# Performance work log

Hardware: AMD Instinct MI355X
Metric: run time of the kernel (lower is better)

The kernel has to match this reference:

```python
import jax, jax.numpy as jnp
import numpy as np

N = 4096      # sequence length (tokens)
D = 256       # model_dim
H = 4         # num_heads
DH = D // H   # dim_per_head = 64
TOPK = 30     # dot_attention default
SCALE = float((DH // H) ** -0.5)  # torch: (key.size(-1)//num_heads)**-0.5 = 16**-0.5 = 0.25
LN_EPS = 1e-5


def setup_inputs() -> dict:
    key = jax.random.key(0)
    ks = jax.random.split(key, 11)
    s = 0.02
    return {
        "key_in":   jax.random.normal(ks[0], (N, D), jnp.float32),
        "value_in": jax.random.normal(ks[1], (N, D), jnp.float32),
        "query_in": jax.random.normal(ks[2], (N, D), jnp.float32),
        "Wq": jax.random.normal(ks[3], (D, D), jnp.float32) * s,
        "bq": jax.random.normal(ks[4], (D,), jnp.float32) * s,
        "Wk": jax.random.normal(ks[5], (D, D), jnp.float32) * s,
        "bk": jax.random.normal(ks[6], (D,), jnp.float32) * s,
        "Wv": jax.random.normal(ks[7], (D, D), jnp.float32) * s,
        "bv": jax.random.normal(ks[8], (D,), jnp.float32) * s,
        "Wo": jax.random.normal(ks[9], (D, D), jnp.float32) * s,
        "bo": jax.random.normal(ks[10], (D,), jnp.float32) * s,
        "ln_g": jnp.ones((D,), jnp.float32),
        "ln_b": jnp.zeros((D,), jnp.float32),
    }


def reference(key_in, value_in, query_in, Wq, bq, Wk, bk, Wv, bv, Wo, bo, ln_g, ln_b):
    # Projections (nn.Linear: x @ W.T + b)
    q = query_in @ Wq.T + bq            # (N, D)
    k = key_in @ Wk.T + bk
    v = value_in @ Wv.T + bv
    # view(N, H, DH).transpose(0,1) -> (H, N, DH)
    qh = q.reshape(N, H, DH).transpose(1, 0, 2)
    kh = k.reshape(N, H, DH).transpose(1, 0, 2)
    vh = v.reshape(N, H, DH).transpose(1, 0, 2)

    scores = jnp.einsum('hnd,hmd->hnm', qh, kh) * SCALE   # (H, N, N)

    # top-k mask via scatter (faithful to torch.topk + scatter_)
    idx = jax.lax.top_k(scores, TOPK)[1]                  # (H, N, TOPK)
    mask = jnp.zeros_like(scores).at[
        jnp.arange(H)[:, None, None],
        jnp.arange(N)[None, :, None],
        idx].set(1.0)
    masked = jnp.where(mask > 0, scores, -jnp.inf)
    attn = jax.nn.softmax(masked, axis=-1)                # (H, N, N); dropout p=0 -> identity

    ctx = jnp.einsum('hnm,hmd->hnd', attn, vh)            # (H, N, DH)
    ctx = ctx.transpose(1, 0, 2).reshape(N, D)

    out = ctx @ Wo.T + bo
    resid = query_in + out                                # residual is pre-projection query
    mu = resid.mean(axis=-1, keepdims=True)
    var = resid.var(axis=-1, keepdims=True)               # biased var, like torch LayerNorm
    out = (resid - mu) / jnp.sqrt(var + LN_EPS) * ln_g + ln_b
    return out, attn
```

## Files before the change

### kernel.cpp

```cpp
#include <hip/hip_runtime.h>
#include <stdint.h>

#define N_TOK 4096
#define DIM   256
#define NH    4
#define DH    64
#define TOPK  30
#define CANDN 40
#define HWIN  128u
#define ATT_SCALE 0.25f
#define LN_EPS 1e-5f

typedef __attribute__((ext_vector_type(8))) short bf16x8;
typedef __attribute__((ext_vector_type(4))) float f32x4;

static __device__ __forceinline__ ushort f2bf(float f) {
    uint x = __float_as_uint(f);
    return (ushort)((x + 0x7FFFu + ((x >> 16) & 1u)) >> 16);
}
static __device__ __forceinline__ bf16x8 load_frag(const ushort* p) {
    union { int4 i; bf16x8 f; } u;
    u.i = *reinterpret_cast<const int4*>(p);
    return u.f;
}
static __device__ __forceinline__ uint s16key(uint u) {
    return (u & 0x8000u) ? (u ^ 0xFFFFu) : (u | 0x8000u);
}
static __device__ __forceinline__ int jdecode(int P) {
    return (P & ~127) | ((P & 7) << 4) | ((P >> 3) & 15);
}

#define BK 32
__global__ __launch_bounds__(256) void qk_gemm_f32(
    const float* __restrict__ query_in, const float* __restrict__ key_in,
    const float* __restrict__ Wq, const float* __restrict__ bq,
    const float* __restrict__ Wk, const float* __restrict__ bk,
    float* __restrict__ qf, float* __restrict__ kf,
    ushort* __restrict__ qb, ushort* __restrict__ kb)
{
    const int j0g = blockIdx.x * 64;
    const int sel = j0g >> 8;
    const int j0  = j0g & 255;
    const float* A    = sel ? key_in : query_in;
    const float* W    = sel ? Wk : Wq;
    const float* bias = sel ? bk : bq;
    float*  outF = sel ? kf : qf;
    ushort* outB = sel ? kb : qb;

    __shared__ float As[BK][64 + 4];
    __shared__ float Ws[BK][64 + 4];
    const int tid = threadIdx.x;
    const int tx = tid & 15;
    const int ty = tid >> 4;
    const int i0 = blockIdx.y * 64;

    float acc[4][4];
#pragma unroll
    for (int r = 0; r < 4; r++)
#pragma unroll
        for (int c = 0; c < 4; c++) acc[r][c] = 0.f;

    for (int k0 = 0; k0 < DIM; k0 += BK) {
#pragma unroll
        for (int u = 0; u < 2; u++) {
            const int f = u * 256 + tid;
            const int r = f >> 3;
            const int c = (f & 7) * 4;
            float4 va = *reinterpret_cast<const float4*>(A + (size_t)(i0 + r) * DIM + k0 + c);
            As[c + 0][r] = va.x; As[c + 1][r] = va.y;
            As[c + 2][r] = va.z; As[c + 3][r] = va.w;
            float4 vw = *reinterpret_cast<const float4*>(W + (size_t)(j0 + r) * DIM + k0 + c);
            Ws[c + 0][r] = vw.x; Ws[c + 1][r] = vw.y;
            Ws[c + 2][r] = vw.z; Ws[c + 3][r] = vw.w;
        }
        __syncthreads();
#pragma unroll
        for (int kk = 0; kk < BK; kk++) {
            const float4 a4 = *reinterpret_cast<const float4*>(&As[kk][ty * 4]);
            const float4 b4 = *reinterpret_cast<const float4*>(&Ws[kk][tx * 4]);
            const float ar[4] = {a4.x, a4.y, a4.z, a4.w};
            const float br[4] = {b4.x, b4.y, b4.z, b4.w};
#pragma unroll
            for (int r = 0; r < 4; r++)
#pragma unroll
                for (int c = 0; c < 4; c++) acc[r][c] += ar[r] * br[c];
        }
        __syncthreads();
    }

#pragma unroll
    for (int r = 0; r < 4; r++) {
        const int gi = i0 + ty * 4 + r;
#pragma unroll
        for (int c = 0; c < 4; c++) {
            const int gj = j0 + tx * 4 + c;
            float v = acc[r][c] + bias[gj];
            outF[(size_t)gi * DIM + gj] = v;
            outB[(size_t)gi * DIM + gj] = f2bf(v);
        }
    }
}

__global__ __launch_bounds__(256) void cast_kernel(
    const float* __restrict__ value_in, const float* __restrict__ Wv,
    const float* __restrict__ Wo, ushort* __restrict__ value_b,
    ushort* __restrict__ Wv_b, ushort* __restrict__ Wo_b)
{
    const int id4 = blockIdx.x * 256 + threadIdx.x;
    const int NV = 1048576 / 4, NW = 65536 / 4;
    const float* src; ushort* dst; int off;
    if (id4 < NV)            { src = value_in; dst = value_b; off = id4; }
    else if (id4 < NV + NW)  { src = Wv; dst = Wv_b; off = id4 - NV; }
    else                     { src = Wo; dst = Wo_b; off = id4 - NV - NW; }
    float4 v = reinterpret_cast<const float4*>(src)[off];
    ushort4 o = {f2bf(v.x), f2bf(v.y), f2bf(v.z), f2bf(v.w)};
    reinterpret_cast<ushort4*>(dst)[off] = o;
}

__global__ __launch_bounds__(256) void mfma_gemm(
    const ushort* __restrict__ A, const ushort* __restrict__ B,
    const float* __restrict__ bias, const float* __restrict__ addX,
    float* __restrict__ outF)
{
    const int lane = threadIdx.x & 63;
    const int wv   = threadIdx.x >> 6;
    const int i0   = blockIdx.y * 64 + wv * 16;
    const int j0   = blockIdx.x * 64;
    const int r = lane & 15, q = lane >> 4;

    f32x4 acc[4];
#pragma unroll
    for (int b = 0; b < 4; b++) acc[b] = (f32x4){0.f, 0.f, 0.f, 0.f};

#pragma unroll
    for (int ks = 0; ks < 8; ks++) {
        const int kk = ks * 32 + q * 8;
        bf16x8 af = load_frag(A + (size_t)(i0 + r) * DIM + kk);
        bf16x8 bfr[4];
#pragma unroll
        for (int jt = 0; jt < 4; jt++)
            bfr[jt] = load_frag(B + (size_t)(j0 + jt * 16 + r) * DIM + kk);
#pragma unroll
        for (int jt = 0; jt < 4; jt++)
            acc[jt] = __builtin_amdgcn_mfma_f32_16x16x32_bf16(af, bfr[jt], acc[jt], 0, 0, 0);
    }

#pragma unroll
    for (int jt = 0; jt < 4; jt++) {
        const int gj = j0 + jt * 16 + r;
        const float bv = bias[gj];
#pragma unroll
        for (int rg = 0; rg < 4; rg++) {
            const int gi = i0 + q * 4 + rg;
            float v = acc[jt][rg] + bv;
            if (addX) v += addX[(size_t)gi * DIM + gj];
            outF[(size_t)gi * DIM + gj] = v;
        }
    }
}

__global__ __launch_bounds__(256) void scores_kernel(
    const ushort* __restrict__ qb, const ushort* __restrict__ kb,
    ushort* __restrict__ sb)
{
    const int lane = threadIdx.x & 63;
    const int wv   = threadIdx.x >> 6;
    const int h    = blockIdx.z;
    const int i0   = blockIdx.y * 128 + wv * 32;
    const int j0   = blockIdx.x * 128;
    const int r = lane & 15, q = lane >> 4;
    const int koff = h * DH;

    f32x4 acc[2][8];
#pragma unroll
    for (int a = 0; a < 2; a++)
#pragma unroll
        for (int b = 0; b < 8; b++) acc[a][b] = (f32x4){0.f, 0.f, 0.f, 0.f};

#pragma unroll
    for (int ks = 0; ks < 2; ks++) {
        const int kk = koff + ks * 32 + q * 8;
        bf16x8 af[2], bfr[8];
#pragma unroll
        for (int mt = 0; mt < 2; mt++)
            af[mt] = load_frag(qb + (size_t)(i0 + mt * 16 + r) * DIM + kk);
#pragma unroll
        for (int jt = 0; jt < 8; jt++)
            bfr[jt] = load_frag(kb + (size_t)(j0 + jt * 16 + r) * DIM + kk);
#pragma unroll
        for (int mt = 0; mt < 2; mt++)
#pragma unroll
            for (int jt = 0; jt < 8; jt++)
                acc[mt][jt] = __builtin_amdgcn_mfma_f32_16x16x32_bf16(
                    af[mt], bfr[jt], acc[mt][jt], 0, 0, 0);
    }

    const int tileBase = (j0 >> 7) * 16;
#pragma unroll
    for (int mt = 0; mt < 2; mt++)
#pragma unroll
        for (int rg = 0; rg < 4; rg++) {
            const int gi = i0 + mt * 16 + q * 4 + rg;
            uint w4[4];
#pragma unroll
            for (int p = 0; p < 4; p++) {
                const uint klo = s16key(f2bf(acc[mt][2 * p + 0][rg]));
                const uint khi = s16key(f2bf(acc[mt][2 * p + 1][rg]));
                w4[p] = klo | (khi << 16);
            }
            int4 outv;
            outv.x = (int)w4[0]; outv.y = (int)w4[1];
            outv.z = (int)w4[2]; outv.w = (int)w4[3];
            int4* rowp = reinterpret_cast<int4*>(sb + ((size_t)(h * N_TOK + gi)) * N_TOK);
            rowp[tileBase + r] = outv;
        }
}

__global__ __launch_bounds__(256) void select_kernel(
    const ushort* __restrict__ sb, const float* __restrict__ qf,
    const float* __restrict__ kf, const float* __restrict__ vf,
    float* __restrict__ pval, int* __restrict__ pidx,
    ushort* __restrict__ ctxb)
{
    const int lane = threadIdx.x & 63;
    const int wv   = threadIdx.x >> 6;
    const int row  = blockIdx.x * 4 + wv;
    const int h    = row >> 12;
    const int i    = row & (N_TOK - 1);
    const ushort* srow = sb + (size_t)row * N_TOK;

    __shared__ uint  hist[4][256];
    __shared__ uint  cand[4][64];
    __shared__ uint  ccnt[4];
    __shared__ float pw[4][TOPK];
    __shared__ int   jw[4][TOPK];
    __shared__ __align__(16) float qsh[4][DH];

    qsh[wv][lane] = qf[(size_t)i * DIM + h * DH + lane];
    if (lane == 0) ccnt[wv] = 0;
#pragma unroll
    for (int b = 0; b < 4; b++) hist[wv][b * 64 + lane] = 0u;

    uint kw[32];
    const int4* srow4 = reinterpret_cast<const int4*>(srow);
#pragma unroll
    for (int t = 0; t < 8; t++) {
        int4 c = srow4[t * 64 + lane];
        kw[t * 4 + 0] = (uint)c.x; kw[t * 4 + 1] = (uint)c.y;
        kw[t * 4 + 2] = (uint)c.z; kw[t * 4 + 3] = (uint)c.w;
    }

    uint mx = 0;
#pragma unroll
    for (int w = 0; w < 32; w++) {
        uint lo16 = kw[w] & 0xFFFFu, hi16 = kw[w] >> 16;
        mx = max(mx, max(lo16, hi16));
    }
#pragma unroll
    for (int off = 32; off; off >>= 1)
        mx = max(mx, (uint)__shfl_xor((int)mx, off));

    __syncthreads();

#pragma unroll
    for (int w = 0; w < 32; w++) {
        uint d0 = mx - (kw[w] & 0xFFFFu);
        uint d1 = mx - (kw[w] >> 16);
        if (d0 < HWIN) atomicAdd(&hist[wv][d0], 1u);
        if (d1 < HWIN) atomicAdd(&hist[wv][d1], 1u);
    }
    __syncthreads();

    const uint c0 = hist[wv][lane * 4 + 0];
    const uint c1 = hist[wv][lane * 4 + 1];
    const uint c2 = hist[wv][lane * 4 + 2];
    const uint c3 = hist[wv][lane * 4 + 3];
    const uint seg = c0 + c1 + c2 + c3;
    uint scan = seg;
#pragma unroll
    for (int d = 1; d < 64; d <<= 1) {
        uint y = (uint)__shfl_up((int)scan, d);
        if (lane >= d) scan += y;
    }
    const uint excl = scan - seg;
    const bool crossing = (excl < CANDN) && (scan >= CANDN);
    unsigned long long bal = __ballot(crossing);

    int t = 256;
    if (bal != 0ull) {
        const int srcLane = __ffsll(bal) - 1;
        int tloc = lane * 4;
        if (crossing) {
            uint cum = excl + c0;
            if (cum < CANDN) { tloc++; cum += c1;
                if (cum < CANDN) { tloc++; cum += c2;
                    if (cum < CANDN) { tloc++; } } }
        }
        t = __shfl(tloc, srcLane);
    }

    uint T;
    if (t <= 254) {
        T = mx - (uint)t;
    } else {
        uint lo = 0;
#pragma unroll
        for (int b = 15; b >= 0; b--) {
            uint trial = lo | (1u << b);
            int c = 0;
#pragma unroll
            for (int w = 0; w < 32; w++) {
                c += ((kw[w] & 0xFFFFu) >= trial) ? 1 : 0;
                c += ((kw[w] >> 16)     >= trial) ? 1 : 0;
            }
#pragma unroll
            for (int off = 32; off; off >>= 1) c += __shfl_xor(c, off);
            if (c >= CANDN) lo = trial;
        }
        T = lo;
    }

#pragma unroll
    for (int w = 0; w < 32; w++) {
        const uint lo16 = kw[w] & 0xFFFFu, hi16 = kw[w] >> 16;
        const int P0 = (w >> 2) * 512 + lane * 8 + (w & 3) * 2;
        if (lo16 >= T) {
            uint pos = atomicAdd(&ccnt[wv], 1u);
            if (pos < 64u) cand[wv][pos] = (uint)jdecode(P0);
        }
        if (hi16 >= T) {
            uint pos = atomicAdd(&ccnt[wv], 1u);
            if (pos < 64u) cand[wv][pos] = (uint)jdecode(P0 + 1);
        }
    }
    __syncthreads();
    const int m = (int)min(ccnt[wv], 64u);

    unsigned long long ukey = 0ull;
    if (lane < m) {
        const int j = (int)cand[wv][lane];
        const float4* kr = reinterpret_cast<const float4*>(kf + (size_t)j * DIM + h * DH);
        const float4* qr = reinterpret_cast<const float4*>(qsh[wv]);
        float s = 0.f;
#pragma unroll
        for (int d = 0; d < 16; d++) {
            float4 a = qr[d], bb = kr[d];
            s += a.x * bb.x; s += a.y * bb.y; s += a.z * bb.z; s += a.w * bb.w;
        }
        uint bits = __float_as_uint(s);
        uint s32 = (bits & 0x80000000u) ? ~bits : (bits | 0x80000000u);
        ukey = ((unsigned long long)s32 << 12) | (unsigned long long)(4095 - j);
    }

#pragma unroll
    for (int k = 2; k <= 64; k <<= 1) {
#pragma unroll
        for (int jj = k >> 1; jj > 0; jj >>= 1) {
            unsigned long long o = __shfl_xor(ukey, jj);
            bool keepMax = ((lane & jj) != 0) ^ ((lane & k) != 0);
            ukey = keepMax ? (ukey > o ? ukey : o) : (ukey < o ? ukey : o);
        }
    }

    const int rank = 63 - lane;
    const int jsel = 4095 - (int)(ukey & 0xFFFull);
    uint s32b = (uint)(ukey >> 12);
    uint fb = (s32b & 0x80000000u) ? (s32b ^ 0x80000000u) : ~s32b;
    const float sc = __uint_as_float(fb);
    const float stop = __shfl(sc, 63);

    float e = (rank < TOPK) ? __expf((sc - stop) * ATT_SCALE) : 0.f;
    float esum = e;
#pragma unroll
    for (int off = 32; off; off >>= 1) esum += __shfl_xor(esum, off);
    const float p = e / esum;

    if (rank < TOPK) {
        pw[wv][rank] = p; jw[wv][rank] = jsel;
        pval[(size_t)row * 32 + rank] = p;
        pidx[(size_t)row * 32 + rank] = jsel;
    }
    __syncthreads();

    float a = 0.f;
#pragma unroll
    for (int c = 0; c < TOPK; c++)
        a += pw[wv][c] * vf[(size_t)jw[wv][c] * DIM + h * DH + lane];
    ctxb[(size_t)i * DIM + h * DH + lane] = f2bf(a);
}

__global__ __launch_bounds__(256) void attn_write(
    const float* __restrict__ pval, const int* __restrict__ pidx,
    float* __restrict__ attnF)
{
    __shared__ __align__(16) float rb[4][N_TOK];
    const int tid = threadIdx.x;
    const int r0 = blockIdx.x * 4;

    float4* rb4 = reinterpret_cast<float4*>(&rb[0][0]);
    const float4 z = {0.f, 0.f, 0.f, 0.f};
#pragma unroll
    for (int t = 0; t < 16; t++) rb4[t * 256 + tid] = z;
    __syncthreads();
    if (tid < 4 * TOPK) {
        const int w = tid / TOPK, c = tid % TOPK;
        rb[w][pidx[(size_t)(r0 + w) * 32 + c]] = pval[(size_t)(r0 + w) * 32 + c];
    }
    __syncthreads();
#pragma unroll
    for (int w = 0; w < 4; w++) {
        float4* grow = reinterpret_cast<float4*>(attnF + (size_t)(r0 + w) * N_TOK);
#pragma unroll
        for (int t = 0; t < 4; t++)
            grow[t * 256 + tid] = rb4[w * 1024 + t * 256 + tid];
    }
}

__global__ __launch_bounds__(64) void ln_kernel(
    float* __restrict__ resb, const float* __restrict__ g,
    const float* __restrict__ b)
{
    const int i = blockIdx.x, lane = threadIdx.x;
    float4* rowp = reinterpret_cast<float4*>(resb + (size_t)i * DIM);
    float4 x = rowp[lane];
    float s  = x.x + x.y + x.z + x.w;
    float sq = x.x * x.x + x.y * x.y + x.z * x.z + x.w * x.w;
#pragma unroll
    for (int off = 32; off; off >>= 1) {
        s  += __shfl_xor(s, off);
        sq += __shfl_xor(sq, off);
    }
    const float mu  = s * (1.f / DIM);
    const float var = sq * (1.f / DIM) - mu * mu;
    const float rstd = rsqrtf(var + LN_EPS);
    const int col = lane * 4;
    float4 o;
    o.x = (x.x - mu) * rstd * g[col + 0] + b[col + 0];
    o.y = (x.y - mu) * rstd * g[col + 1] + b[col + 1];
    o.z = (x.z - mu) * rstd * g[col + 2] + b[col + 2];
    o.w = (x.w - mu) * rstd * g[col + 3] + b[col + 3];
    rowp[lane] = o;
}

extern "C" void kernel_launch(void* const* d_in, const int* in_sizes, int n_in,
                              void* d_out, int out_size, void* d_ws, size_t ws_size,
                              hipStream_t stream)
{
    const float* key_in   = (const float*)d_in[0];
    const float* value_in = (const float*)d_in[1];
    const float* query_in = (const float*)d_in[2];
    const float* Wq = (const float*)d_in[3];
    const float* bq = (const float*)d_in[4];
    const float* Wk = (const float*)d_in[5];
    const float* bk = (const float*)d_in[6];
    const float* Wv = (const float*)d_in[7];
    const float* bv = (const float*)d_in[8];
    const float* Wo = (const float*)d_in[9];
    const float* bo = (const float*)d_in[10];
    const float* ln_g = (const float*)d_in[11];
    const float* ln_b = (const float*)d_in[12];

    float* outF  = (float*)d_out;
    float* attnF = outF + (size_t)N_TOK * DIM;

    const size_t SC = 33554432;
    ushort* sb   = (ushort*)attnF;
    float*  qf   = attnF + SC;
    float*  kf   = attnF + SC + 1048576;
    float*  vf   = attnF + SC + 2097152;
    ushort* qb   = (ushort*)(attnF + SC + 3145728);
    ushort* kb   = (ushort*)(attnF + SC + 3670016);
    ushort* ctxb = (ushort*)(attnF + SC + 4194304);

    float*  pval    = (float*)d_ws;
    int*    pidx    = (int*)d_ws + 524288;
    ushort* value_b = (ushort*)((char*)d_ws + (4u << 20));
    ushort* Wv_b    = (ushort*)((char*)d_ws + (6u << 20));
    ushort* Wo_b    = (ushort*)((char*)d_ws + (6u << 20) + 131072);

    cast_kernel<<<dim3((1048576 + 65536 + 65536) / 4 / 256), 256, 0, stream>>>(
        value_in, Wv, Wo, value_b, Wv_b, Wo_b);
    qk_gemm_f32<<<dim3(8, 64), 256, 0, stream>>>(
        query_in, key_in, Wq, bq, Wk, bk, qf, kf, qb, kb);
    mfma_gemm<<<dim3(4, 64), 256, 0, stream>>>(value_b, Wv_b, bv, nullptr, vf);

    scores_kernel<<<dim3(32, 32, NH), 256, 0, stream>>>(qb, kb, sb);
    select_kernel<<<dim3(N_TOK * NH / 4), 256, 0, stream>>>(
        sb, qf, kf, vf, pval, pidx, ctxb);

    mfma_gemm<<<dim3(4, 64), 256, 0, stream>>>(ctxb, Wo_b, bo, query_in, outF);
    ln_kernel<<<N_TOK, 64, 0, stream>>>(outF, ln_g, ln_b);

    attn_write<<<N_TOK * NH / 4, 256, 0, stream>>>(pval, pidx, attnF);
}
```

Measured before the change: 443.1 us.

## Fuse projections, cast, and LayerNorm into fewer kernel launches

Removes the standalone bf16 cast kernel by converting value_in, Wv and Wo to bf16 on the fly inside the MFMA GEMMs. The Q/K fp32 GEMM and the V projection now share one launch, split by block index, and LayerNorm is folded into the attention-write kernel as extra blocks. This saves three launches and the cast kernel's round trip through memory. In exchange, the GEMMs now read fp32 operands, which doubles their load bytes and repeats the conversion per tile.

```diff
diff --git a/kernel.cpp b/kernel.cpp
--- a/kernel.cpp
+++ b/kernel.cpp
@@ -23,6 +23,14 @@
     u.i = *reinterpret_cast<const int4*>(p);
     return u.f;
 }
+static __device__ __forceinline__ bf16x8 cvt_frag(const float* p) {
+    float4 a = *reinterpret_cast<const float4*>(p);
+    float4 b = *reinterpret_cast<const float4*>(p + 4);
+    union { ushort u[8]; bf16x8 f; } u;
+    u.u[0] = f2bf(a.x); u.u[1] = f2bf(a.y); u.u[2] = f2bf(a.z); u.u[3] = f2bf(a.w);
+    u.u[4] = f2bf(b.x); u.u[5] = f2bf(b.y); u.u[6] = f2bf(b.z); u.u[7] = f2bf(b.w);
+    return u.f;
+}
 static __device__ __forceinline__ uint s16key(uint u) {
     return (u & 0x8000u) ? (u ^ 0xFFFFu) : (u | 0x8000u);
 }
@@ -31,94 +39,117 @@
 }
 
 #define BK 32
-__global__ __launch_bounds__(256) void qk_gemm_f32(
+__global__ __launch_bounds__(256) void front_kernel(
     const float* __restrict__ query_in, const float* __restrict__ key_in,
+    const float* __restrict__ value_in,
     const float* __restrict__ Wq, const float* __restrict__ bq,
     const float* __restrict__ Wk, const float* __restrict__ bk,
+    const float* __restrict__ Wv, const float* __restrict__ bv,
     float* __restrict__ qf, float* __restrict__ kf,
-    ushort* __restrict__ qb, ushort* __restrict__ kb)
+    ushort* __restrict__ qb, ushort* __restrict__ kb,
+    float* __restrict__ vf)
 {
-    const int j0g = blockIdx.x * 64;
-    const int sel = j0g >> 8;
-    const int j0  = j0g & 255;
-    const float* A    = sel ? key_in : query_in;
-    const float* W    = sel ? Wk : Wq;
-    const float* bias = sel ? bk : bq;
-    float*  outF = sel ? kf : qf;
-    ushort* outB = sel ? kb : qb;
-
-    __shared__ float As[BK][64 + 4];
-    __shared__ float Ws[BK][64 + 4];
-    const int tid = threadIdx.x;
-    const int tx = tid & 15;
-    const int ty = tid >> 4;
-    const int i0 = blockIdx.y * 64;
-
-    float acc[4][4];
-#pragma unroll
-    for (int r = 0; r < 4; r++)
-#pragma unroll
-        for (int c = 0; c < 4; c++) acc[r][c] = 0.f;
-
-    for (int k0 = 0; k0 < DIM; k0 += BK) {
-#pragma unroll
-        for (int u = 0; u < 2; u++) {
-            const int f = u * 256 + tid;
-            const int r = f >> 3;
-            const int c = (f & 7) * 4;
-            float4 va = *reinterpret_cast<const float4*>(A + (size_t)(i0 + r) * DIM + k0 + c);
-            As[c + 0][r] = va.x; As[c + 1][r] = va.y;
-            As[c + 2][r] = va.z; As[c + 3][r] = va.w;
-            float4 vw = *reinterpret_cast<const float4*>(W + (size_t)(j0 + r) * DIM + k0 + c);
-            Ws[c + 0][r] = vw.x; Ws[c + 1][r] = vw.y;
-            Ws[c + 2][r] = vw.z; Ws[c + 3][r] = vw.w;
-        }
-        __syncthreads();
-#pragma unroll
-        for (int kk = 0; kk < BK; kk++) {
-            const float4 a4 = *reinterpret_cast<const float4*>(&As[kk][ty * 4]);
-            const float4 b4 = *reinterpret_cast<const float4*>(&Ws[kk][tx * 4]);
-            const float ar[4] = {a4.x, a4.y, a4.z, a4.w};
-            const float br[4] = {b4.x, b4.y, b4.z, b4.w};
-#pragma unroll
-            for (int r = 0; r < 4; r++)
-#pragma unroll
-                for (int c = 0; c < 4; c++) acc[r][c] += ar[r] * br[c];
-        }
-        __syncthreads();
-    }
-
-#pragma unroll
-    for (int r = 0; r < 4; r++) {
-        const int gi = i0 + ty * 4 + r;
-#pragma unroll
-        for (int c = 0; c < 4; c++) {
-            const int gj = j0 + tx * 4 + c;
-            float v = acc[r][c] + bias[gj];
-            outF[(size_t)gi * DIM + gj] = v;
-            outB[(size_t)gi * DIM + gj] = f2bf(v);
-        }
-    }
-}
-
-__global__ __launch_bounds__(256) void cast_kernel(
-    const float* __restrict__ value_in, const float* __restrict__ Wv,
-    const float* __restrict__ Wo, ushort* __restrict__ value_b,
-    ushort* __restrict__ Wv_b, ushort* __restrict__ Wo_b)
-{
-    const int id4 = blockIdx.x * 256 + threadIdx.x;
-    const int NV = 1048576 / 4, NW = 65536 / 4;
-    const float* src; ushort* dst; int off;
-    if (id4 < NV)            { src = value_in; dst = value_b; off = id4; }
-    else if (id4 < NV + NW)  { src = Wv; dst = Wv_b; off = id4 - NV; }
-    else                     { src = Wo; dst = Wo_b; off = id4 - NV - NW; }
-    float4 v = reinterpret_cast<const float4*>(src)[off];
-    ushort4 o = {f2bf(v.x), f2bf(v.y), f2bf(v.z), f2bf(v.w)};
-    reinterpret_cast<ushort4*>(dst)[off] = o;
-}
-
-__global__ __launch_bounds__(256) void mfma_gemm(
-    const ushort* __restrict__ A, const ushort* __restrict__ B,
+    if (blockIdx.x < 8) {
+        const int j0g = blockIdx.x * 64;
+        const int sel = j0g >> 8;
+        const int j0  = j0g & 255;
+        const float* A    = sel ? key_in : query_in;
+        const float* W    = sel ? Wk : Wq;
+        const float* bias = sel ? bk : bq;
+        float*  outF = sel ? kf : qf;
+        ushort* outB = sel ? kb : qb;
+
+        __shared__ float As[BK][64 + 4];
+        __shared__ float Ws[BK][64 + 4];
+        const int tid = threadIdx.x;
+        const int tx = tid & 15;
+        const int ty = tid >> 4;
+        const int i0 = blockIdx.y * 64;
+
+        float acc[4][4];
+#pragma unroll
+        for (int r = 0; r < 4; r++)
+#pragma unroll
+            for (int c = 0; c < 4; c++) acc[r][c] = 0.f;
+
+        for (int k0 = 0; k0 < DIM; k0 += BK) {
+#pragma unroll
+            for (int u = 0; u < 2; u++) {
+                const int f = u * 256 + tid;
+                const int r = f >> 3;
+                const int c = (f & 7) * 4;
+                float4 va = *reinterpret_cast<const float4*>(A + (size_t)(i0 + r) * DIM + k0 + c);
+                As[c + 0][r] = va.x; As[c + 1][r] = va.y;
+                As[c + 2][r] = va.z; As[c + 3][r] = va.w;
+                float4 vw = *reinterpret_cast<const float4*>(W + (size_t)(j0 + r) * DIM + k0 + c);
+                Ws[c + 0][r] = vw.x; Ws[c + 1][r] = vw.y;
+                Ws[c + 2][r] = vw.z; Ws[c + 3][r] = vw.w;
+            }
+            __syncthreads();
+#pragma unroll
+            for (int kk = 0; kk < BK; kk++) {
+                const float4 a4 = *reinterpret_cast<const float4*>(&As[kk][ty * 4]);
+                const float4 b4 = *reinterpret_cast<const float4*>(&Ws[kk][tx * 4]);
+                const float ar[4] = {a4.x, a4.y, a4.z, a4.w};
+                const float br[4] = {b4.x, b4.y, b4.z, b4.w};
+#pragma unroll
+                for (int r = 0; r < 4; r++)
+#pragma unroll
+                    for (int c = 0; c < 4; c++) acc[r][c] += ar[r] * br[c];
+            }
+            __syncthreads();
+        }
+
+#pragma unroll
+        for (int r = 0; r < 4; r++) {
+            const int gi = i0 + ty * 4 + r;
+#pragma unroll
+            for (int c = 0; c < 4; c++) {
+                const int gj = j0 + tx * 4 + c;
+                float v = acc[r][c] + bias[gj];
+                outF[(size_t)gi * DIM + gj] = v;
+                outB[(size_t)gi * DIM + gj] = f2bf(v);
+            }
+        }
+    } else {
+        const int lane = threadIdx.x & 63;
+        const int wv   = threadIdx.x >> 6;
+        const int i0   = blockIdx.y * 64 + wv * 16;
+        const int j0   = (blockIdx.x - 8) * 64;
+        const int r = lane & 15, q = lane >> 4;
+
+        f32x4 acc[4];
+#pragma unroll
+        for (int b = 0; b < 4; b++) acc[b] = (f32x4){0.f, 0.f, 0.f, 0.f};
+
+#pragma unroll
+        for (int ks = 0; ks < 8; ks++) {
+            const int kk = ks * 32 + q * 8;
+            bf16x8 af = cvt_frag(value_in + (size_t)(i0 + r) * DIM + kk);
+            bf16x8 bfr[4];
+#pragma unroll
+            for (int jt = 0; jt < 4; jt++)
+                bfr[jt] = cvt_frag(Wv + (size_t)(j0 + jt * 16 + r) * DIM + kk);
+#pragma unroll
+            for (int jt = 0; jt < 4; jt++)
+                acc[jt] = __builtin_amdgcn_mfma_f32_16x16x32_bf16(af, bfr[jt], acc[jt], 0, 0, 0);
+        }
+
+#pragma unroll
+        for (int jt = 0; jt < 4; jt++) {
+            const int gj = j0 + jt * 16 + r;
+            const float bvv = bv[gj];
+#pragma unroll
+            for (int rg = 0; rg < 4; rg++) {
+                const int gi = i0 + q * 4 + rg;
+                vf[(size_t)gi * DIM + gj] = acc[jt][rg] + bvv;
+            }
+        }
+    }
+}
+
+__global__ __launch_bounds__(256) void oproj_kernel(
+    const ushort* __restrict__ A, const float* __restrict__ Wo,
     const float* __restrict__ bias, const float* __restrict__ addX,
     float* __restrict__ outF)
 {
@@ -139,7 +170,7 @@
         bf16x8 bfr[4];
 #pragma unroll
         for (int jt = 0; jt < 4; jt++)
-            bfr[jt] = load_frag(B + (size_t)(j0 + jt * 16 + r) * DIM + kk);
+            bfr[jt] = cvt_frag(Wo + (size_t)(j0 + jt * 16 + r) * DIM + kk);
 #pragma unroll
         for (int jt = 0; jt < 4; jt++)
             acc[jt] = __builtin_amdgcn_mfma_f32_16x16x32_bf16(af, bfr[jt], acc[jt], 0, 0, 0);
@@ -148,12 +179,11 @@
 #pragma unroll
     for (int jt = 0; jt < 4; jt++) {
         const int gj = j0 + jt * 16 + r;
-        const float bv = bias[gj];
+        const float bvv = bias[gj];
 #pragma unroll
         for (int rg = 0; rg < 4; rg++) {
             const int gi = i0 + q * 4 + rg;
-            float v = acc[jt][rg] + bv;
-            if (addX) v += addX[(size_t)gi * DIM + gj];
+            float v = acc[jt][rg] + bvv + addX[(size_t)gi * DIM + gj];
             outF[(size_t)gi * DIM + gj] = v;
         }
     }
@@ -389,57 +419,59 @@
     ctxb[(size_t)i * DIM + h * DH + lane] = f2bf(a);
 }
 
-__global__ __launch_bounds__(256) void attn_write(
+__global__ __launch_bounds__(256) void attn_ln(
     const float* __restrict__ pval, const int* __restrict__ pidx,
-    float* __restrict__ attnF)
+    float* __restrict__ attnF,
+    float* __restrict__ resb, const float* __restrict__ g,
+    const float* __restrict__ b)
 {
     __shared__ __align__(16) float rb[4][N_TOK];
     const int tid = threadIdx.x;
-    const int r0 = blockIdx.x * 4;
-
-    float4* rb4 = reinterpret_cast<float4*>(&rb[0][0]);
-    const float4 z = {0.f, 0.f, 0.f, 0.f};
-#pragma unroll
-    for (int t = 0; t < 16; t++) rb4[t * 256 + tid] = z;
-    __syncthreads();
-    if (tid < 4 * TOPK) {
-        const int w = tid / TOPK, c = tid % TOPK;
-        rb[w][pidx[(size_t)(r0 + w) * 32 + c]] = pval[(size_t)(r0 + w) * 32 + c];
-    }
-    __syncthreads();
-#pragma unroll
-    for (int w = 0; w < 4; w++) {
-        float4* grow = reinterpret_cast<float4*>(attnF + (size_t)(r0 + w) * N_TOK);
-#pragma unroll
-        for (int t = 0; t < 4; t++)
-            grow[t * 256 + tid] = rb4[w * 1024 + t * 256 + tid];
-    }
-}
-
-__global__ __launch_bounds__(64) void ln_kernel(
-    float* __restrict__ resb, const float* __restrict__ g,
-    const float* __restrict__ b)
-{
-    const int i = blockIdx.x, lane = threadIdx.x;
-    float4* rowp = reinterpret_cast<float4*>(resb + (size_t)i * DIM);
-    float4 x = rowp[lane];
-    float s  = x.x + x.y + x.z + x.w;
-    float sq = x.x * x.x + x.y * x.y + x.z * x.z + x.w * x.w;
-#pragma unroll
-    for (int off = 32; off; off >>= 1) {
-        s  += __shfl_xor(s, off);
-        sq += __shfl_xor(sq, off);
-    }
-    const float mu  = s * (1.f / DIM);
-    const float var = sq * (1.f / DIM) - mu * mu;
-    const float rstd = rsqrtf(var + LN_EPS);
-    const int col = lane * 4;
-    float4 o;
-    o.x = (x.x - mu) * rstd * g[col + 0] + b[col + 0];
-    o.y = (x.y - mu) * rstd * g[col + 1] + b[col + 1];
-    o.z = (x.z - mu) * rstd * g[col + 2] + b[col + 2];
-    o.w = (x.w - mu) * rstd * g[col + 3] + b[col + 3];
-    rowp[lane] = o;
+
+    if (blockIdx.x < 4096) {
+        const int r0 = blockIdx.x * 4;
+
+        float4* rb4 = reinterpret_cast<float4*>(&rb[0][0]);
+        const float4 z = {0.f, 0.f, 0.f, 0.f};
+#pragma unroll
+        for (int t = 0; t < 16; t++) rb4[t * 256 + tid] = z;
+        __syncthreads();
+        if (tid < 4 * TOPK) {
+            const int w = tid / TOPK, c = tid % TOPK;
+            rb[w][pidx[(size_t)(r0 + w) * 32 + c]] = pval[(size_t)(r0 + w) * 32 + c];
+        }
+        __syncthreads();
+#pragma unroll
+        for (int w = 0; w < 4; w++) {
+            float4* grow = reinterpret_cast<float4*>(attnF + (size_t)(r0 + w) * N_TOK);
+#pragma unroll
+            for (int t = 0; t < 4; t++)
+                grow[t * 256 + tid] = rb4[w * 1024 + t * 256 + tid];
+        }
+    } else {
+        const int lane = tid & 63;
+        const int wv   = tid >> 6;
+        const int i    = (blockIdx.x - 4096) * 4 + wv;
+        float4* rowp = reinterpret_cast<float4*>(resb + (size_t)i * DIM);
+        float4 x = rowp[lane];
+        float s  = x.x + x.y + x.z + x.w;
+        float sq = x.x * x.x + x.y * x.y + x.z * x.z + x.w * x.w;
+#pragma unroll
+        for (int off = 32; off; off >>= 1) {
+            s  += __shfl_xor(s, off);
+            sq += __shfl_xor(sq, off);
+        }
+        const float mu  = s * (1.f / DIM);
+        const float var = sq * (1.f / DIM) - mu * mu;
+        const float rstd = rsqrtf(var + LN_EPS);
+        const int col = lane * 4;
+        float4 o;
+        o.x = (x.x - mu) * rstd * g[col + 0] + b[col + 0];
+        o.y = (x.y - mu) * rstd * g[col + 1] + b[col + 1];
+        o.z = (x.z - mu) * rstd * g[col + 2] + b[col + 2];
+        o.w = (x.w - mu) * rstd * g[col + 3] + b[col + 3];
+        rowp[lane] = o;
+    }
 }
 
 extern "C" void kernel_launch(void* const* d_in, const int* in_sizes, int n_in,
@@ -474,22 +506,17 @@
 
     float*  pval    = (float*)d_ws;
     int*    pidx    = (int*)d_ws + 524288;
-    ushort* value_b = (ushort*)((char*)d_ws + (4u << 20));
-    ushort* Wv_b    = (ushort*)((char*)d_ws + (6u << 20));
-    ushort* Wo_b    = (ushort*)((char*)d_ws + (6u << 20) + 131072);
-
-    cast_kernel<<<dim3((1048576 + 65536 + 65536) / 4 / 256), 256, 0, stream>>>(
-        value_in, Wv, Wo, value_b, Wv_b, Wo_b);
-    qk_gemm_f32<<<dim3(8, 64), 256, 0, stream>>>(
-        query_in, key_in, Wq, bq, Wk, bk, qf, kf, qb, kb);
-    mfma_gemm<<<dim3(4, 64), 256, 0, stream>>>(value_b, Wv_b, bv, nullptr, vf);
+
+    front_kernel<<<dim3(12, 64), 256, 0, stream>>>(
+        query_in, key_in, value_in, Wq, bq, Wk, bk, Wv, bv,
+        qf, kf, qb, kb, vf);
 
     scores_kernel<<<dim3(32, 32, NH), 256, 0, stream>>>(qb, kb, sb);
     select_kernel<<<dim3(N_TOK * NH / 4), 256, 0, stream>>>(
         sb, qf, kf, vf, pval, pidx, ctxb);
 
-    mfma_gemm<<<dim3(4, 64), 256, 0, stream>>>(ctxb, Wo_b, bo, query_in, outF);
-    ln_kernel<<<N_TOK, 64, 0, stream>>>(outF, ln_g, ln_b);
-
-    attn_write<<<N_TOK * NH / 4, 256, 0, stream>>>(pval, pidx, attnF);
-}
+    oproj_kernel<<<dim3(4, 64), 256, 0, stream>>>(ctxb, Wo, bo, query_in, outF);
+
+    attn_ln<<<dim3(4096 + 1024), 256, 0, stream>>>(
+        pval, pidx, attnF, outF, ln_g, ln_b);
+}
```

New measurement: 439.0 us. No clear change (-0.9%).
